# Kernel tuning notes

Measured on AMD Instinct MI355X. Metric: run time of the kernel, lower is better.

## Reference

```python
import jax, jax.numpy as jnp
import numpy as np

T, B, N_IN, N_RNN, N_OUT = 1000, 128, 85, 512, 33
ALPHA = 0.2
SIGMA = float(np.sqrt(2.0 / ALPHA) * 0.05)  # sqrt(2/alpha) * sigma_rec


def setup_inputs() -> dict:
    key = jax.random.key(0)
    k_x, k_win, k_wout, k_noise = jax.random.split(key, 4)
    x = jax.random.normal(k_x, (T, B, N_IN), dtype=jnp.float32)
    # weight = concat(w_in0, w_rec0) along axis 0, per LeakyRNNCell init
    w_in0 = jax.random.normal(k_win, (N_IN, N_RNN), dtype=jnp.float32) / np.sqrt(N_IN)  # _w_in_start=1.0
    w_rec0 = 0.5 * jnp.eye(N_RNN, dtype=jnp.float32)  # 'diag' init, _w_rec_start=0.5 (softplus)
    W = jnp.concatenate([w_in0, w_rec0], axis=0)  # [N_IN+N_RNN, N_RNN]
    b = jnp.zeros((N_RNN,), dtype=jnp.float32)
    W_out = jax.random.normal(k_wout, (N_RNN, N_OUT), dtype=jnp.float32) / np.sqrt(N_RNN)
    b_out = jnp.zeros((N_OUT,), dtype=jnp.float32)
    # recurrent noise randn_like(state)*sigma, precomputed for all timesteps
    noise = jax.random.normal(k_noise, (T, B, N_RNN), dtype=jnp.float32) * SIGMA
    return {"x": x, "W": W, "b": b, "W_out": W_out, "b_out": b_out, "noise": noise}


def reference(x, W, b, W_out, b_out, noise):
    # Leaky RNN: h_t = (1-alpha)*h_{t-1} + alpha*softplus([x_t, h_{t-1}] @ W + b + noise_t)
    def step(state, xs):
        x_t, n_t = xs
        gate = jnp.concatenate([x_t, state], axis=1) @ W + b + n_t  # [B, N_RNN]
        out = (1.0 - ALPHA) * state + ALPHA * jax.nn.softplus(gate)
        return out, out

    state0 = jnp.zeros((x.shape[1], W.shape[1]), dtype=x.dtype)
    _, h = jax.lax.scan(step, state0, (x, noise))  # h: [T, B, N_RNN]
    y_hat = jax.nn.sigmoid(h @ W_out + b_out)  # lsq loss head: [T, B, N_OUT]
    return y_hat, h
```

## Files before the change

### kernel.cpp

```cpp
#include <hip/hip_runtime.h>
#include <cmath>

#define T_STEPS 1000
#define B_SZ    128
#define N_IN    85
#define N_RNN   512
#define N_OUT   33
#define K_PAD   88
#define Y_SIZE  (T_STEPS * B_SZ * N_OUT)

__global__ void k_zero_flag(int* flag) {
    if (threadIdx.x == 0 && blockIdx.x == 0) *flag = 0;
}

__global__ void k_check_diag(const float* __restrict__ W, int* flag) {
    const float* Wr = W + N_IN * N_RNN;
    bool bad = false;
    for (int i = blockIdx.x * blockDim.x + threadIdx.x;
         i < N_RNN * N_RNN; i += gridDim.x * blockDim.x) {
        int r = i >> 9, c = i & (N_RNN - 1);
        float v = Wr[i];
        if (r != c && v != 0.0f) bad = true;
    }
    if (bad) atomicOr(flag, 1);
}

__global__ __launch_bounds__(256) void k_precompute(
        const float* __restrict__ x, const float* __restrict__ W,
        const float* __restrict__ bias, const float* __restrict__ noise,
        float* __restrict__ G) {
    __shared__ float xs[128 * K_PAD];
    const int tid = threadIdx.x;
    const int n   = ((blockIdx.x & 1) << 8) + tid;
    const int r0  = (blockIdx.x >> 1) << 7;

    float wcol[K_PAD];
    #pragma unroll
    for (int k = 0; k < N_IN; ++k) wcol[k] = W[k * N_RNN + n];
    wcol[85] = 0.f; wcol[86] = 0.f; wcol[87] = 0.f;

    const float* xsrc = x + (size_t)r0 * N_IN;
    for (int i = tid; i < 128 * K_PAD; i += 256) {
        const int r = i / K_PAD;
        const int k = i - r * K_PAD;
        xs[i] = (k < N_IN) ? xsrc[r * N_IN + k] : 0.0f;
    }
    const float bn = bias[n];
    __syncthreads();

    for (int rb = 0; rb < 16; ++rb) {
        const int rbase = rb << 3;
        const size_t gbase = (size_t)(r0 + rbase) * N_RNN + n;
        float np[8];
        #pragma unroll
        for (int rr = 0; rr < 8; ++rr) np[rr] = noise[gbase + (size_t)rr * N_RNN];
        float acc[8] = {0.f, 0.f, 0.f, 0.f, 0.f, 0.f, 0.f, 0.f};
        #pragma unroll
        for (int k4 = 0; k4 < K_PAD / 4; ++k4) {
            const float w0 = wcol[4 * k4 + 0];
            const float w1 = wcol[4 * k4 + 1];
            const float w2 = wcol[4 * k4 + 2];
            const float w3 = wcol[4 * k4 + 3];
            #pragma unroll
            for (int rr = 0; rr < 8; ++rr) {
                const float4 xv = *(const float4*)&xs[(rbase + rr) * K_PAD + 4 * k4];
                acc[rr] = fmaf(xv.x, w0, acc[rr]);
                acc[rr] = fmaf(xv.y, w1, acc[rr]);
                acc[rr] = fmaf(xv.z, w2, acc[rr]);
                acc[rr] = fmaf(xv.w, w3, acc[rr]);
            }
        }
        #pragma unroll
        for (int rr = 0; rr < 8; ++rr) {
            G[gbase + (size_t)rr * N_RNN] = acc[rr] + bn + np[rr];
        }
    }
}

__device__ __forceinline__ float softplus_f(float g) {
    return fmaxf(g, 0.0f) + __logf(1.0f + __expf(-fabsf(g)));
}

__global__ __launch_bounds__(128) void k_scan_fast(const float* __restrict__ W,
                                                   float* __restrict__ GH,
                                                   const int* __restrict__ flag) {
    if (*flag != 0) return;
    const int b  = blockIdx.x >> 2;
    const int n  = ((blockIdx.x & 3) << 7) + threadIdx.x;
    const int strideT = B_SZ * N_RNN;
    float* base = GH + b * N_RNN + n;
    const float dn = W[(N_IN + n) * N_RNN + n];
    float h = 0.0f;

    float ring[16];
    #pragma unroll
    for (int i = 0; i < 16; ++i) ring[i] = base[i * strideT];
    #pragma unroll 1
    for (int tb = 0; tb < 62; ++tb) {
        const int t0 = tb << 4;
        #pragma unroll
        for (int u = 0; u < 16; ++u) {
            const int t = t0 + u;
            float g = ring[u] + dn * h;
            const int tp = t + 16;
            if (tp < T_STEPS) ring[u] = base[tp * strideT];
            const float sp = softplus_f(g);
            h = 0.8f * h + 0.2f * sp;
            base[t * strideT] = h;
        }
    }
    #pragma unroll
    for (int u = 0; u < 8; ++u) {
        const int t = 992 + u;
        float g = ring[u] + dn * h;
        const float sp = softplus_f(g);
        h = 0.8f * h + 0.2f * sp;
        base[t * strideT] = h;
    }
}

__global__ __launch_bounds__(512) void k_scan_general(const float* __restrict__ W,
                                                      float* __restrict__ GH,
                                                      const int* __restrict__ flag) {
    if (*flag == 0) return;
    const int b = blockIdx.x;
    const int n = threadIdx.x;
    const int strideT = B_SZ * N_RNN;
    float* base = GH + b * N_RNN + n;
    float h = 0.0f;
    __shared__ float hs[N_RNN];
    const float* Wr = W + N_IN * N_RNN;
    for (int t = 0; t < T_STEPS; ++t) {
        hs[n] = h;
        __syncthreads();
        float g = base[t * strideT];
        for (int k = 0; k < N_RNN; ++k) {
            g = fmaf(hs[k], Wr[k * N_RNN + n], g);
        }
        const float sp = softplus_f(g);
        h = 0.8f * h + 0.2f * sp;
        base[t * strideT] = h;
        __syncthreads();
    }
}

__global__ __launch_bounds__(256) void k_head(const float* __restrict__ hbase,
                                              const float* __restrict__ Wout,
                                              const float* __restrict__ bout,
                                              float* __restrict__ y) {
    __shared__ float ws[N_RNN][36];
    __shared__ float bs[64];
    const int tid = threadIdx.x;
    for (int i = tid; i < N_RNN * N_OUT; i += 256) {
        int k = i / N_OUT;
        int o = i - k * N_OUT;
        ws[k][o] = Wout[i];
    }
    if (tid < N_OUT) bs[tid] = bout[tid];
    __syncthreads();

    const int row = blockIdx.x * 256 + tid;
    const float* hr = hbase + (size_t)row * N_RNN;
    float acc[N_OUT];
    #pragma unroll
    for (int o = 0; o < N_OUT; ++o) acc[o] = bs[o];

    for (int k4 = 0; k4 < N_RNN / 4; ++k4) {
        const float4 hv = *(const float4*)(hr + 4 * k4);
        const float* w0 = &ws[4 * k4][0];
        #pragma unroll
        for (int j = 0; j < 4; ++j) {
            const float hx = (j == 0) ? hv.x : (j == 1) ? hv.y : (j == 2) ? hv.z : hv.w;
            const float4* wr = (const float4*)(w0 + j * 36);
            #pragma unroll
            for (int oo = 0; oo < 8; ++oo) {
                const float4 wv = wr[oo];
                acc[4 * oo + 0] = fmaf(hx, wv.x, acc[4 * oo + 0]);
                acc[4 * oo + 1] = fmaf(hx, wv.y, acc[4 * oo + 1]);
                acc[4 * oo + 2] = fmaf(hx, wv.z, acc[4 * oo + 2]);
                acc[4 * oo + 3] = fmaf(hx, wv.w, acc[4 * oo + 3]);
            }
            acc[32] = fmaf(hx, w0[j * 36 + 32], acc[32]);
        }
    }
    float* yr = y + (size_t)row * N_OUT;
    #pragma unroll
    for (int o = 0; o < N_OUT; ++o) {
        yr[o] = 1.0f / (1.0f + __expf(-acc[o]));
    }
}

extern "C" void kernel_launch(void* const* d_in, const int* in_sizes, int n_in,
                              void* d_out, int out_size, void* d_ws, size_t ws_size,
                              hipStream_t stream) {
    const float* x     = (const float*)d_in[0];
    const float* W     = (const float*)d_in[1];
    const float* bias  = (const float*)d_in[2];
    const float* Wout  = (const float*)d_in[3];
    const float* bout  = (const float*)d_in[4];
    const float* noise = (const float*)d_in[5];

    float* y  = (float*)d_out;
    float* GH = y + Y_SIZE;
    int* flag = (int*)d_out;

    k_zero_flag<<<1, 64, 0, stream>>>(flag);
    k_check_diag<<<256, 256, 0, stream>>>(W, flag);
    k_precompute<<<2000, 256, 0, stream>>>(x, W, bias, noise, GH);
    k_scan_fast<<<512, 128, 0, stream>>>(W, GH, flag);
    k_scan_general<<<128, 512, 0, stream>>>(W, GH, flag);
    k_head<<<500, 256, 0, stream>>>(GH, Wout, bout, y);
}
```

Baseline: 1.100 ms.

## Fuse input projection into diagonal recurrent scan kernel to skip gate buffer

```diff
diff --git a/kernel.cpp b/kernel.cpp
--- a/kernel.cpp
+++ b/kernel.cpp
@@ -25,11 +25,113 @@
     if (bad) atomicOr(flag, 1);
 }
 
+__device__ __forceinline__ float softplus_f(float g) {
+    return fmaxf(g, 0.0f) + __logf(1.0f + __expf(-fabsf(g)));
+}
+
+__global__ __launch_bounds__(128) void k_scan_fused(
+        const float* __restrict__ x, const float* __restrict__ W,
+        const float* __restrict__ bias, const float* __restrict__ noise,
+        float* __restrict__ H, const int* __restrict__ flag) {
+    if (*flag != 0) return;
+    const int tid = threadIdx.x;
+    const int b   = blockIdx.x >> 2;
+    const int n   = ((blockIdx.x & 3) << 7) + tid;
+
+    float wcol[K_PAD];
+    #pragma unroll
+    for (int k = 0; k < N_IN; ++k) wcol[k] = W[k * N_RNN + n];
+    wcol[85] = 0.f; wcol[86] = 0.f; wcol[87] = 0.f;
+    const float dn = W[(N_IN + n) * N_RNN + n];
+    const float bn = bias[n];
+
+    __shared__ __align__(16) float xs[2][8][K_PAD];
+    const int row = tid >> 4;
+    const int l16 = tid & 15;
+
+    const size_t strT = (size_t)B_SZ * N_RNN;
+    const float* np = noise + (size_t)b * N_RNN + n;
+    float*       hp = H     + (size_t)b * N_RNN + n;
+
+    float rA[8], rB[8], xr[6];
+    float h = 0.0f;
+
+    auto XLD = [&](int t0) {
+        const int t = t0 + row;
+        const float* xrow = x + ((size_t)t * B_SZ + b) * N_IN;
+        #pragma unroll
+        for (int j = 0; j < 6; ++j) {
+            const int k = l16 + 16 * j;
+            xr[j] = (t < T_STEPS && k < N_IN) ? xrow[k] : 0.0f;
+        }
+    };
+    auto XST = [&](int buf) {
+        #pragma unroll
+        for (int j = 0; j < 6; ++j) {
+            const int k = l16 + 16 * j;
+            if (k < K_PAD) xs[buf][row][k] = xr[j];
+        }
+    };
+    auto pref8 = [&](float (&ring)[8], int t0) {
+        #pragma unroll
+        for (int u = 0; u < 8; ++u) ring[u] = np[(size_t)(t0 + u) * strT];
+    };
+    auto consume8 = [&](float (&ring)[8], int t0, int buf) {
+        #pragma unroll
+        for (int u = 0; u < 8; ++u) {
+            const float4* xv4 = (const float4*)(&xs[buf][u][0]);
+            float a0 = 0.f, a1 = 0.f, a2 = 0.f, a3 = 0.f;
+            #pragma unroll
+            for (int k4 = 0; k4 < K_PAD / 4; ++k4) {
+                const float4 xv = xv4[k4];
+                a0 = fmaf(xv.x, wcol[4 * k4 + 0], a0);
+                a1 = fmaf(xv.y, wcol[4 * k4 + 1], a1);
+                a2 = fmaf(xv.z, wcol[4 * k4 + 2], a2);
+                a3 = fmaf(xv.w, wcol[4 * k4 + 3], a3);
+            }
+            const float g = ((a0 + a1) + (a2 + a3)) + (bn + ring[u]) + dn * h;
+            h = 0.8f * h + 0.2f * softplus_f(g);
+            hp[(size_t)(t0 + u) * strT] = h;
+        }
+    };
+
+    pref8(rA, 0);
+    XLD(0); XST(0);
+    XLD(8);
+    asm volatile("s_waitcnt lgkmcnt(0)" ::: "memory");
+    __builtin_amdgcn_s_barrier();
+    __builtin_amdgcn_sched_barrier(0);
+
+    int cur = 0;
+    #pragma unroll 1
+    for (int tb2 = 0; tb2 < 62; ++tb2) {
+        const int bb = tb2 << 1;
+        pref8(rB, (bb + 1) << 3);
+        consume8(rA, bb << 3, cur);
+        XST(cur ^ 1);
+        XLD((bb + 2) << 3);
+        asm volatile("s_waitcnt lgkmcnt(0)" ::: "memory");
+        __builtin_amdgcn_s_barrier();
+        __builtin_amdgcn_sched_barrier(0);
+        cur ^= 1;
+        pref8(rA, (bb + 2) << 3);
+        consume8(rB, (bb + 1) << 3, cur);
+        XST(cur ^ 1);
+        XLD((bb + 3) << 3);
+        asm volatile("s_waitcnt lgkmcnt(0)" ::: "memory");
+        __builtin_amdgcn_s_barrier();
+        __builtin_amdgcn_sched_barrier(0);
+        cur ^= 1;
+    }
+    consume8(rA, 992, cur);
+}
+
 __global__ __launch_bounds__(256) void k_precompute(
         const float* __restrict__ x, const float* __restrict__ W,
         const float* __restrict__ bias, const float* __restrict__ noise,
-        float* __restrict__ G) {
-    __shared__ float xs[128 * K_PAD];
+        float* __restrict__ G, const int* __restrict__ flag) {
+    if (*flag == 0) return;
+    __shared__ float xsh[128 * K_PAD];
     const int tid = threadIdx.x;
     const int n   = ((blockIdx.x & 1) << 8) + tid;
     const int r0  = (blockIdx.x >> 1) << 7;
@@ -43,7 +145,7 @@
     for (int i = tid; i < 128 * K_PAD; i += 256) {
         const int r = i / K_PAD;
         const int k = i - r * K_PAD;
-        xs[i] = (k < N_IN) ? xsrc[r * N_IN + k] : 0.0f;
+        xsh[i] = (k < N_IN) ? xsrc[r * N_IN + k] : 0.0f;
     }
     const float bn = bias[n];
     __syncthreads();
@@ -51,9 +153,9 @@
     for (int rb = 0; rb < 16; ++rb) {
         const int rbase = rb << 3;
         const size_t gbase = (size_t)(r0 + rbase) * N_RNN + n;
-        float np[8];
-        #pragma unroll
-        for (int rr = 0; rr < 8; ++rr) np[rr] = noise[gbase + (size_t)rr * N_RNN];
+        float npv[8];
+        #pragma unroll
+        for (int rr = 0; rr < 8; ++rr) npv[rr] = noise[gbase + (size_t)rr * N_RNN];
         float acc[8] = {0.f, 0.f, 0.f, 0.f, 0.f, 0.f, 0.f, 0.f};
         #pragma unroll
         for (int k4 = 0; k4 < K_PAD / 4; ++k4) {
@@ -63,7 +165,7 @@
             const float w3 = wcol[4 * k4 + 3];
             #pragma unroll
             for (int rr = 0; rr < 8; ++rr) {
-                const float4 xv = *(const float4*)&xs[(rbase + rr) * K_PAD + 4 * k4];
+                const float4 xv = *(const float4*)&xsh[(rbase + rr) * K_PAD + 4 * k4];
                 acc[rr] = fmaf(xv.x, w0, acc[rr]);
                 acc[rr] = fmaf(xv.y, w1, acc[rr]);
                 acc[rr] = fmaf(xv.z, w2, acc[rr]);
@@ -72,50 +174,8 @@
         }
         #pragma unroll
         for (int rr = 0; rr < 8; ++rr) {
-            G[gbase + (size_t)rr * N_RNN] = acc[rr] + bn + np[rr];
-        }
-    }
-}
-
-__device__ __forceinline__ float softplus_f(float g) {
-    return fmaxf(g, 0.0f) + __logf(1.0f + __expf(-fabsf(g)));
-}
-
-__global__ __launch_bounds__(128) void k_scan_fast(const float* __restrict__ W,
-                                                   float* __restrict__ GH,
-                                                   const int* __restrict__ flag) {
-    if (*flag != 0) return;
-    const int b  = blockIdx.x >> 2;
-    const int n  = ((blockIdx.x & 3) << 7) + threadIdx.x;
-    const int strideT = B_SZ * N_RNN;
-    float* base = GH + b * N_RNN + n;
-    const float dn = W[(N_IN + n) * N_RNN + n];
-    float h = 0.0f;
-
-    float ring[16];
-    #pragma unroll
-    for (int i = 0; i < 16; ++i) ring[i] = base[i * strideT];
-    #pragma unroll 1
-    for (int tb = 0; tb < 62; ++tb) {
-        const int t0 = tb << 4;
-        #pragma unroll
-        for (int u = 0; u < 16; ++u) {
-            const int t = t0 + u;
-            float g = ring[u] + dn * h;
-            const int tp = t + 16;
-            if (tp < T_STEPS) ring[u] = base[tp * strideT];
-            const float sp = softplus_f(g);
-            h = 0.8f * h + 0.2f * sp;
-            base[t * strideT] = h;
-        }
-    }
-    #pragma unroll
-    for (int u = 0; u < 8; ++u) {
-        const int t = 992 + u;
-        float g = ring[u] + dn * h;
-        const float sp = softplus_f(g);
-        h = 0.8f * h + 0.2f * sp;
-        base[t * strideT] = h;
+            G[gbase + (size_t)rr * N_RNN] = acc[rr] + bn + npv[rr];
+        }
     }
 }
 
@@ -206,8 +266,8 @@
 
     k_zero_flag<<<1, 64, 0, stream>>>(flag);
     k_check_diag<<<256, 256, 0, stream>>>(W, flag);
-    k_precompute<<<2000, 256, 0, stream>>>(x, W, bias, noise, GH);
-    k_scan_fast<<<512, 128, 0, stream>>>(W, GH, flag);
+    k_scan_fused<<<512, 128, 0, stream>>>(x, W, bias, noise, GH, flag);
+    k_precompute<<<2000, 256, 0, stream>>>(x, W, bias, noise, GH, flag);
     k_scan_general<<<128, 512, 0, stream>>>(W, GH, flag);
     k_head<<<500, 256, 0, stream>>>(GH, Wout, bout, y);
 }
```

Measured after the change: 997.5 us. 1.1x faster.
